# Performance work log

Measured on AMD Instinct MI355X. Metric: run time of the kernel, lower is better.

Reference implementation:

```python
import jax, jax.numpy as jnp
import numpy as np

Q_HEADS, KV_HEADS, HEAD_SIZE, H, MAX_LEN = 16, 4, 64, 1024, 4096
B, S = 1, 4096


def _rope_tables(max_len, head_size):
    half = head_size // 2
    inv_freq = 1.0 / (10000.0 ** (np.arange(half, dtype=np.float32) / half))
    pos = np.arange(max_len, dtype=np.float32)
    ang = pos[:, None] * inv_freq[None, :]  # [max_len, half]
    return jnp.asarray(np.sin(ang)), jnp.asarray(np.cos(ang))


def setup_inputs() -> dict:
    key = jax.random.key(0)
    ks = jax.random.split(key, 6)
    sc = 1.0 / np.sqrt(H)
    x = jax.random.normal(ks[0], (B, S, H), dtype=jnp.float32)
    wq = jax.random.normal(ks[1], (H, H), dtype=jnp.float32) * sc
    wk = jax.random.normal(ks[2], (H, KV_HEADS * HEAD_SIZE), dtype=jnp.float32) * sc
    wv = jax.random.normal(ks[3], (H, KV_HEADS * HEAD_SIZE), dtype=jnp.float32) * sc
    wo = jax.random.normal(ks[4], (H, H), dtype=jnp.float32) * sc
    sin, cos = _rope_tables(MAX_LEN, HEAD_SIZE)
    full_mask = jnp.tril(jnp.ones((MAX_LEN, MAX_LEN), dtype=bool))
    attention_mask = jnp.ones((B, S), dtype=jnp.int32)
    return {"x": x, "attention_mask": attention_mask, "start": 0,
            "wq": wq, "wk": wk, "wv": wv, "wo": wo,
            "sin": sin, "cos": cos, "full_mask": full_mask}


def _rotate(t, sin, cos, start):
    # t: [b, heads, s, head_size]; interleaved even/odd RoPE
    s = t.shape[2]
    sn = sin[start:start + s, :][None, None, :, :]
    cs = cos[start:start + s, :][None, None, :, :]
    even, odd = t[..., 0::2], t[..., 1::2]
    out_even = cs * even - sn * odd
    out_odd = sn * even + cs * odd
    return jnp.stack((out_even, out_odd), axis=-1).reshape(t.shape)


def _expand_kv(t, group):
    # [b, kv_heads, s, d] -> [b, kv_heads*group, s, d]
    b, kvh, s, d = t.shape
    return jnp.broadcast_to(t[:, :, None], (b, kvh, group, s, d)).reshape(b, kvh * group, s, d)


def reference(x, attention_mask, start, wq, wk, wv, wo, sin, cos, full_mask):
    b, s, _ = x.shape
    group = Q_HEADS // KV_HEADS
    Q = (x @ wq).reshape(b, s, Q_HEADS, HEAD_SIZE).transpose(0, 2, 1, 3)
    K = (x @ wk).reshape(b, s, KV_HEADS, HEAD_SIZE).transpose(0, 2, 1, 3)
    V = (x @ wv).reshape(b, s, KV_HEADS, HEAD_SIZE).transpose(0, 2, 1, 3)
    Q = _rotate(Q, sin, cos, start)
    K = _rotate(K, sin, cos, start)
    K = _expand_kv(K, group)
    V = _expand_kv(V, group)
    z = jnp.einsum('bhqd,bhkd->bhqk', Q, K) / (HEAD_SIZE ** 0.5)
    kv_len = start + s
    mask = full_mask[:s, :kv_len][None, None, :, :]
    amask = (attention_mask[:, :kv_len] != 0)[:, None, None, :]
    mask = mask & amask
    z = jnp.where(mask, z, -1000000.0)
    A = jax.nn.softmax(z, axis=-1)
    ctx = jnp.einsum('bhqk,bhkd->bhqd', A, V)
    q_mask = attention_mask[:, :s].astype(ctx.dtype)[:, None, :, None]
    ctx = ctx * q_mask
    ctx = ctx.transpose(0, 2, 1, 3).reshape(b, s, H)
    return ctx @ wo
```

## Files before the change

### kernel.cpp

```cpp
#include <hip/hip_runtime.h>

typedef __bf16 bf16x8 __attribute__((ext_vector_type(8)));
typedef float f32x4 __attribute__((ext_vector_type(4)));
typedef unsigned int u32x4 __attribute__((ext_vector_type(4)));

typedef const void __attribute__((address_space(1)))* gas1;
typedef void __attribute__((address_space(3)))* las3;

__device__ __forceinline__ unsigned short f2bf(float f) {
  unsigned int u = __builtin_bit_cast(unsigned int, f);
  u += 0x7fffu + ((u >> 16) & 1u);
  return (unsigned short)(u >> 16);
}
__device__ __forceinline__ float bf2f(unsigned short h) {
  unsigned int u = ((unsigned int)h) << 16;
  return __builtin_bit_cast(float, u);
}
__device__ __forceinline__ unsigned int pack2bf(float lo, float hi) {
  return (unsigned int)f2bf(lo) | ((unsigned int)f2bf(hi) << 16);
}
__device__ __forceinline__ unsigned int packtr(float lo, float hi) {
  return __builtin_amdgcn_perm(__builtin_bit_cast(unsigned int, hi),
                               __builtin_bit_cast(unsigned int, lo), 0x07060302u);
}

__global__ __launch_bounds__(256) void cvt_f32_bf16(const float* __restrict__ src,
                                                    unsigned short* __restrict__ dst, int n4) {
  int i = blockIdx.x * 256 + threadIdx.x;
  if (i >= n4) return;
  float4 v = ((const float4*)src)[i];
  uint2 o;
  o.x = pack2bf(v.x, v.y);
  o.y = pack2bf(v.z, v.w);
  ((uint2*)dst)[i] = o;
}

__global__ __launch_bounds__(256) void transpose_cvt(const float* __restrict__ src,
                                                     unsigned short* __restrict__ dst,
                                                     int R, int C) {
  __shared__ float tile[32][33];
  int c0 = blockIdx.x * 32, r0 = blockIdx.y * 32;
  int tx = threadIdx.x & 31, ty = threadIdx.x >> 5;
#pragma unroll
  for (int i = 0; i < 4; ++i)
    tile[ty + i * 8][tx] = src[(r0 + ty + i * 8) * C + c0 + tx];
  __syncthreads();
#pragma unroll
  for (int i = 0; i < 4; ++i)
    dst[(c0 + ty + i * 8) * R + r0 + tx] = f2bf(tile[tx][ty + i * 8]);
}

__global__ __launch_bounds__(256, 2) void gemm_bt2(const unsigned short* __restrict__ A,
                                                   const unsigned short* __restrict__ Bt,
                                                   void* __restrict__ Cout,
                                                   int M, int N, int K, int outF32) {
  __shared__ __align__(16) unsigned short Als[128 * 32];
  __shared__ __align__(16) unsigned short Bls[128 * 32];
  const int tid = threadIdx.x;
  const int wave = tid >> 6, lane = tid & 63;
  const int lgrp = lane >> 4, lmod = lane & 15;
  const int wm = (wave & 1) * 64, wn = (wave >> 1) * 64;
  const int m0 = blockIdx.y * 128, n0 = blockIdx.x * 128;

  f32x4 acc[4][4] = {};

  for (int k0 = 0; k0 < K; k0 += 32) {
    __syncthreads();
#pragma unroll
    for (int it = 0; it < 2; ++it) {
      int idx = tid + it * 256;
      int rr = idx >> 2, cc = (idx & 3) * 8;
      __builtin_amdgcn_global_load_lds((gas1)(const void*)&A[(size_t)(m0 + rr) * K + k0 + cc],
                                       (las3)(void*)&Als[(it * 256 + wave * 64) * 8], 16, 0, 0);
      __builtin_amdgcn_global_load_lds((gas1)(const void*)&Bt[(size_t)(n0 + rr) * K + k0 + cc],
                                       (las3)(void*)&Bls[(it * 256 + wave * 64) * 8], 16, 0, 0);
    }
    __syncthreads();
    bf16x8 af[4], bfr[4];
#pragma unroll
    for (int mi = 0; mi < 4; ++mi)
      af[mi] = __builtin_bit_cast(bf16x8, *(const u32x4*)&Als[(wm + mi * 16 + lmod) * 32 + lgrp * 8]);
#pragma unroll
    for (int ni = 0; ni < 4; ++ni)
      bfr[ni] = __builtin_bit_cast(bf16x8, *(const u32x4*)&Bls[(wn + ni * 16 + lmod) * 32 + lgrp * 8]);
#pragma unroll
    for (int mi = 0; mi < 4; ++mi)
#pragma unroll
      for (int ni = 0; ni < 4; ++ni)
        acc[mi][ni] = __builtin_amdgcn_mfma_f32_16x16x32_bf16(af[mi], bfr[ni], acc[mi][ni], 0, 0, 0);
  }

#pragma unroll
  for (int mi = 0; mi < 4; ++mi)
#pragma unroll
    for (int ni = 0; ni < 4; ++ni)
#pragma unroll
      for (int r = 0; r < 4; ++r) {
        int row = m0 + wm + mi * 16 + lgrp * 4 + r;
        int col = n0 + wn + ni * 16 + lmod;
        float v = acc[mi][ni][r];
        if (outF32) ((float*)Cout)[row * N + col] = v;
        else ((unsigned short*)Cout)[row * N + col] = f2bf(v);
      }
}

__global__ __launch_bounds__(256) void rope_split(const unsigned short* __restrict__ qkv,
                                                  const float* __restrict__ sinT,
                                                  const float* __restrict__ cosT,
                                                  unsigned short* __restrict__ Qh,
                                                  unsigned short* __restrict__ Kh) {
  const float qscale = 0.18033688011112042f;
  int p = blockIdx.x * 256 + threadIdx.x;
  int s = p / 640, cp = p % 640;
  int col = cp * 2;
  unsigned int pair = *(const unsigned int*)&qkv[s * 1536 + col];
  float e = bf2f((unsigned short)(pair & 0xffff));
  float o = bf2f((unsigned short)(pair >> 16));
  if (col < 1024) {
    int h = col >> 6, d = col & 63, i = d >> 1;
    float sn = sinT[s * 32 + i], cs = cosT[s * 32 + i];
    unsigned int w = pack2bf((cs * e - sn * o) * qscale, (sn * e + cs * o) * qscale);
    *(unsigned int*)&Qh[(h * 4096 + s) * 64 + d] = w;
  } else {
    int c = col - 1024;
    int h = c >> 6, d = c & 63, i = d >> 1;
    float sn = sinT[s * 32 + i], cs = cosT[s * 32 + i];
    unsigned int w = pack2bf(cs * e - sn * o, sn * e + cs * o);
    *(unsigned int*)&Kh[(h * 4096 + s) * 64 + d] = w;
  }
}

__global__ __launch_bounds__(256) void transpose_v(const unsigned short* __restrict__ qkv,
                                                   unsigned short* __restrict__ Vt) {
  __shared__ unsigned short tile[32][33];
  int h = blockIdx.z;
  int d0 = blockIdx.y * 32;
  int s0 = blockIdx.x * 32;
  int tx = threadIdx.x & 31, ty = threadIdx.x >> 5;
#pragma unroll
  for (int i = 0; i < 4; ++i)
    tile[ty + i * 8][tx] = qkv[(s0 + ty + i * 8) * 1536 + 1280 + h * 64 + d0 + tx];
  __syncthreads();
#pragma unroll
  for (int i = 0; i < 4; ++i)
    Vt[(h * 64 + d0 + ty + i * 8) * 4096 + s0 + tx] = tile[tx][ty + i * 8];
}

__global__ __launch_bounds__(256, 2) void attn3(const unsigned short* __restrict__ Qh,
                                                const unsigned short* __restrict__ Kh,
                                                const unsigned short* __restrict__ Vt,
                                                unsigned short* __restrict__ ctx) {
  __shared__ __align__(16) unsigned short Kls[128 * 68];
  __shared__ __align__(16) unsigned short Vls[64 * 136];
  const int bx = blockIdx.x;
  const int head = bx & 15;
  const int qidx = bx >> 4;
  const int qb = (qidx < 16) ? (31 - qidx) : (qidx - 16);
  const int kvh = head >> 2;
  const int tid = threadIdx.x;
  const int wave = tid >> 6, lane = tid & 63;
  const int lgrp = lane >> 4, lmod = lane & 15;
  const int qbase = qb * 128;

  const unsigned short* Kg = Kh + (size_t)kvh * 4096 * 64;
  const unsigned short* Vg = Vt + (size_t)kvh * 64 * 4096;

  bf16x8 qf[2][2];
  int qrow[2];
#pragma unroll
  for (int qt = 0; qt < 2; ++qt) {
    qrow[qt] = qbase + wave * 32 + qt * 16 + lmod;
    const unsigned short* Qg = Qh + ((size_t)head * 4096 + qrow[qt]) * 64;
    qf[qt][0] = __builtin_bit_cast(bf16x8, *(const u32x4*)&Qg[lgrp * 8]);
    qf[qt][1] = __builtin_bit_cast(bf16x8, *(const u32x4*)&Qg[32 + lgrp * 8]);
  }

  const int kbase = (8 * (lmod >> 2) + (lmod & 3)) * 68 + lgrp * 8;
  const int vbase = lmod * 136 + lgrp * 8;

  f32x4 accO[2][4] = {};
  float m_i[2] = {-3e38f, -3e38f}, l_i[2] = {0.f, 0.f};

  for (int kc = 0; kc <= qb; ++kc) {
    const int kb = kc * 128;
    __syncthreads();
#pragma unroll
    for (int i = 0; i < 4; ++i) {
      int ii = tid + i * 256;
      int r = ii >> 3, sg = (ii & 7) * 8;
      u32x4 dK = *(const u32x4*)&Kg[(size_t)(kb + r) * 64 + sg];
      uint2* pd = (uint2*)&Kls[r * 68 + sg];
      pd[0] = make_uint2(dK[0], dK[1]);
      pd[1] = make_uint2(dK[2], dK[3]);
    }
#pragma unroll
    for (int i = 0; i < 4; ++i) {
      int ii = tid + i * 256;
      int r = ii >> 4, sg = (ii & 15) * 8;
      *(u32x4*)&Vls[r * 136 + sg] = *(const u32x4*)&Vg[(size_t)r * 4096 + kb + sg];
    }
    __syncthreads();

    f32x4 s[4][2][2];
#pragma unroll
    for (int g = 0; g < 4; ++g)
#pragma unroll
      for (int t = 0; t < 2; ++t) {
        const unsigned short* ka = &Kls[kbase + (32 * g + 4 * t) * 68];
        uint2 a0 = *(const uint2*)&ka[0];
        uint2 a1 = *(const uint2*)&ka[4];
        uint2 b0 = *(const uint2*)&ka[32];
        uint2 b1 = *(const uint2*)&ka[36];
        u32x4 lo = {a0.x, a0.y, a1.x, a1.y};
        u32x4 hi = {b0.x, b0.y, b1.x, b1.y};
        bf16x8 alo = __builtin_bit_cast(bf16x8, lo);
        bf16x8 ahi = __builtin_bit_cast(bf16x8, hi);
#pragma unroll
        for (int qt = 0; qt < 2; ++qt) {
          f32x4 z = {};
          z = __builtin_amdgcn_mfma_f32_16x16x32_bf16(alo, qf[qt][0], z, 0, 0, 0);
          z = __builtin_amdgcn_mfma_f32_16x16x32_bf16(ahi, qf[qt][1], z, 0, 0, 0);
          s[g][t][qt] = z;
        }
      }

#pragma unroll
    for (int qt = 0; qt < 2; ++qt) {
      if (kb + 127 > qbase + wave * 32 + qt * 16) {
#pragma unroll
        for (int g = 0; g < 4; ++g)
#pragma unroll
          for (int t = 0; t < 2; ++t)
#pragma unroll
            for (int r = 0; r < 4; ++r) {
              int key = kb + 32 * g + 8 * lgrp + 4 * t + r;
              if (key > qrow[qt]) s[g][t][qt][r] = -3e38f;
            }
      }
    }

#pragma unroll
    for (int qt = 0; qt < 2; ++qt) {
      f32x4 v0 = s[0][0][qt], v1 = s[0][1][qt];
#pragma unroll
      for (int g = 1; g < 4; ++g)
#pragma unroll
        for (int r = 0; r < 4; ++r) {
          v0[r] = fmaxf(v0[r], s[g][0][qt][r]);
          v1[r] = fmaxf(v1[r], s[g][1][qt][r]);
        }
      float mx = fmaxf(fmaxf(fmaxf(v0[0], v0[1]), fmaxf(v0[2], v0[3])),
                       fmaxf(fmaxf(v1[0], v1[1]), fmaxf(v1[2], v1[3])));
      mx = fmaxf(mx, __shfl_xor(mx, 16, 64));
      mx = fmaxf(mx, __shfl_xor(mx, 32, 64));
      float mnew = fmaxf(m_i[qt], mx);
      float alpha = __builtin_amdgcn_exp2f(m_i[qt] - mnew);
      m_i[qt] = mnew;
      f32x4 su = {};
#pragma unroll
      for (int g = 0; g < 4; ++g)
#pragma unroll
        for (int t = 0; t < 2; ++t)
#pragma unroll
          for (int r = 0; r < 4; ++r) {
            float ev = __builtin_amdgcn_exp2f(s[g][t][qt][r] - mnew);
            s[g][t][qt][r] = ev;
            su[r] += ev;
          }
      float rs = (su[0] + su[1]) + (su[2] + su[3]);
      rs += __shfl_xor(rs, 16, 64);
      rs += __shfl_xor(rs, 32, 64);
      l_i[qt] = l_i[qt] * alpha + rs;
#pragma unroll
      for (int dt = 0; dt < 4; ++dt)
#pragma unroll
        for (int r = 0; r < 4; ++r) accO[qt][dt][r] *= alpha;
    }

#pragma unroll
    for (int g = 0; g < 4; ++g) {
      bf16x8 pf[2];
#pragma unroll
      for (int qt = 0; qt < 2; ++qt) {
        u32x4 pk;
        pk[0] = packtr(s[g][0][qt][0], s[g][0][qt][1]);
        pk[1] = packtr(s[g][0][qt][2], s[g][0][qt][3]);
        pk[2] = packtr(s[g][1][qt][0], s[g][1][qt][1]);
        pk[3] = packtr(s[g][1][qt][2], s[g][1][qt][3]);
        pf[qt] = __builtin_bit_cast(bf16x8, pk);
      }
#pragma unroll
      for (int dt = 0; dt < 4; ++dt) {
        bf16x8 vf = __builtin_bit_cast(bf16x8, *(const u32x4*)&Vls[vbase + dt * 2176 + 32 * g]);
        accO[0][dt] = __builtin_amdgcn_mfma_f32_16x16x32_bf16(vf, pf[0], accO[0][dt], 0, 0, 0);
        accO[1][dt] = __builtin_amdgcn_mfma_f32_16x16x32_bf16(vf, pf[1], accO[1][dt], 0, 0, 0);
      }
    }
  }

#pragma unroll
  for (int qt = 0; qt < 2; ++qt) {
    float inv = 1.f / l_i[qt];
#pragma unroll
    for (int dt = 0; dt < 4; ++dt) {
      uint2 o;
      o.x = pack2bf(accO[qt][dt][0] * inv, accO[qt][dt][1] * inv);
      o.y = pack2bf(accO[qt][dt][2] * inv, accO[qt][dt][3] * inv);
      *(uint2*)&ctx[(size_t)qrow[qt] * 1024 + head * 64 + dt * 16 + lgrp * 4] = o;
    }
  }
}

extern "C" void kernel_launch(void* const* d_in, const int* in_sizes, int n_in,
                              void* d_out, int out_size, void* d_ws, size_t ws_size,
                              hipStream_t stream) {
  const float* x    = (const float*)d_in[0];
  const float* wq   = (const float*)d_in[3];
  const float* wk   = (const float*)d_in[4];
  const float* wv   = (const float*)d_in[5];
  const float* wo   = (const float*)d_in[6];
  const float* sinT = (const float*)d_in[7];
  const float* cosT = (const float*)d_in[8];

  unsigned short* ws    = (unsigned short*)d_ws;
  unsigned short* xb    = ws;
  unsigned short* wtqkv = xb + 4096 * 1024;
  unsigned short* wot   = wtqkv + 1536 * 1024;
  unsigned short* qkv   = wot + 1024 * 1024;
  unsigned short* Qh    = qkv + 4096 * 1536;
  unsigned short* Kh    = Qh + 16 * 4096 * 64;
  unsigned short* Vt    = Kh + 4 * 4096 * 64;
  unsigned short* ctx   = Vt + 4 * 64 * 4096;
  float* out = (float*)d_out;

  cvt_f32_bf16<<<4096, 256, 0, stream>>>(x, xb, 4096 * 1024 / 4);
  transpose_cvt<<<dim3(32, 32), 256, 0, stream>>>(wq, wtqkv, 1024, 1024);
  transpose_cvt<<<dim3(8, 32), 256, 0, stream>>>(wk, wtqkv + 1024 * 1024, 1024, 256);
  transpose_cvt<<<dim3(8, 32), 256, 0, stream>>>(wv, wtqkv + 1280 * 1024, 1024, 256);
  transpose_cvt<<<dim3(32, 32), 256, 0, stream>>>(wo, wot, 1024, 1024);

  gemm_bt2<<<dim3(12, 32), 256, 0, stream>>>(xb, wtqkv, qkv, 4096, 1536, 1024, 0);

  rope_split<<<10240, 256, 0, stream>>>(qkv, sinT, cosT, Qh, Kh);
  transpose_v<<<dim3(128, 2, 4), 256, 0, stream>>>(qkv, Vt);

  attn3<<<dim3(512), 256, 0, stream>>>(Qh, Kh, Vt, ctx);

  gemm_bt2<<<dim3(8, 32), 256, 0, stream>>>(ctx, wot, out, 4096, 1024, 1024, 1);
}
```

Measured before the change: 269.5 us.

## Split causal attention KV ranges across blocks with combine pass; smaller GEMM tiles

Attention now splits each query block's causal key range into up to four segments, so the grid grows from 512 to 1280 blocks with more even per-block work. A new combine kernel merges the partial outputs using the saved max and sum values. The GEMMs switch to 64x128 tiles with 128-thread blocks to launch more blocks. In exchange, partial results take an extra global write and read, and Opart reuses the xb workspace region.

```diff
diff --git a/kernel.cpp b/kernel.cpp
--- a/kernel.cpp
+++ b/kernel.cpp
@@ -50,17 +50,18 @@
     dst[(c0 + ty + i * 8) * R + r0 + tx] = f2bf(tile[tx][ty + i * 8]);
 }
 
-__global__ __launch_bounds__(256, 2) void gemm_bt2(const unsigned short* __restrict__ A,
-                                                   const unsigned short* __restrict__ Bt,
-                                                   void* __restrict__ Cout,
-                                                   int M, int N, int K, int outF32) {
-  __shared__ __align__(16) unsigned short Als[128 * 32];
+__global__ __launch_bounds__(128) void gemm_bt3(const unsigned short* __restrict__ A,
+                                                const unsigned short* __restrict__ Bt,
+                                                void* __restrict__ Cout,
+                                                int M, int N, int K, int outF32) {
+  __shared__ __align__(16) unsigned short Als[64 * 32];
   __shared__ __align__(16) unsigned short Bls[128 * 32];
   const int tid = threadIdx.x;
   const int wave = tid >> 6, lane = tid & 63;
   const int lgrp = lane >> 4, lmod = lane & 15;
-  const int wm = (wave & 1) * 64, wn = (wave >> 1) * 64;
-  const int m0 = blockIdx.y * 128, n0 = blockIdx.x * 128;
+  const int wn = wave * 64;
+  const int m0 = blockIdx.y * 64, n0 = blockIdx.x * 128;
+  const int lr = lane >> 2, lc = (lane & 3) * 8;
 
   f32x4 acc[4][4] = {};
 
@@ -68,18 +69,23 @@
     __syncthreads();
 #pragma unroll
     for (int it = 0; it < 2; ++it) {
-      int idx = tid + it * 256;
-      int rr = idx >> 2, cc = (idx & 3) * 8;
-      __builtin_amdgcn_global_load_lds((gas1)(const void*)&A[(size_t)(m0 + rr) * K + k0 + cc],
-                                       (las3)(void*)&Als[(it * 256 + wave * 64) * 8], 16, 0, 0);
-      __builtin_amdgcn_global_load_lds((gas1)(const void*)&Bt[(size_t)(n0 + rr) * K + k0 + cc],
-                                       (las3)(void*)&Bls[(it * 256 + wave * 64) * 8], 16, 0, 0);
+      int idx = wave * 2 + it;
+      __builtin_amdgcn_global_load_lds(
+          (gas1)(const void*)&A[(size_t)(m0 + idx * 16 + lr) * K + k0 + lc],
+          (las3)(void*)&Als[idx * 512], 16, 0, 0);
+    }
+#pragma unroll
+    for (int it = 0; it < 4; ++it) {
+      int idx = wave * 4 + it;
+      __builtin_amdgcn_global_load_lds(
+          (gas1)(const void*)&Bt[(size_t)(n0 + idx * 16 + lr) * K + k0 + lc],
+          (las3)(void*)&Bls[idx * 512], 16, 0, 0);
     }
     __syncthreads();
     bf16x8 af[4], bfr[4];
 #pragma unroll
     for (int mi = 0; mi < 4; ++mi)
-      af[mi] = __builtin_bit_cast(bf16x8, *(const u32x4*)&Als[(wm + mi * 16 + lmod) * 32 + lgrp * 8]);
+      af[mi] = __builtin_bit_cast(bf16x8, *(const u32x4*)&Als[(mi * 16 + lmod) * 32 + lgrp * 8]);
 #pragma unroll
     for (int ni = 0; ni < 4; ++ni)
       bfr[ni] = __builtin_bit_cast(bf16x8, *(const u32x4*)&Bls[(wn + ni * 16 + lmod) * 32 + lgrp * 8]);
@@ -96,11 +102,11 @@
     for (int ni = 0; ni < 4; ++ni)
 #pragma unroll
       for (int r = 0; r < 4; ++r) {
-        int row = m0 + wm + mi * 16 + lgrp * 4 + r;
+        int row = m0 + mi * 16 + lgrp * 4 + r;
         int col = n0 + wn + ni * 16 + lmod;
         float v = acc[mi][ni][r];
-        if (outF32) ((float*)Cout)[row * N + col] = v;
-        else ((unsigned short*)Cout)[row * N + col] = f2bf(v);
+        if (outF32) ((float*)Cout)[(size_t)row * N + col] = v;
+        else ((unsigned short*)Cout)[(size_t)row * N + col] = f2bf(v);
       }
 }
 
@@ -146,16 +152,29 @@
     Vt[(h * 64 + d0 + ty + i * 8) * 4096 + s0 + tx] = tile[tx][ty + i * 8];
 }
 
-__global__ __launch_bounds__(256, 2) void attn3(const unsigned short* __restrict__ Qh,
+__global__ __launch_bounds__(256, 2) void attn4(const unsigned short* __restrict__ Qh,
                                                 const unsigned short* __restrict__ Kh,
                                                 const unsigned short* __restrict__ Vt,
-                                                unsigned short* __restrict__ ctx) {
+                                                unsigned short* __restrict__ Opart,
+                                                float2* __restrict__ ML) {
   __shared__ __align__(16) unsigned short Kls[128 * 68];
   __shared__ __align__(16) unsigned short Vls[64 * 136];
-  const int bx = blockIdx.x;
-  const int head = bx & 15;
-  const int qidx = bx >> 4;
-  const int qb = (qidx < 16) ? (31 - qidx) : (qidx - 16);
+  const int head = blockIdx.y;
+  const int r = 79 - blockIdx.x;
+  int g, base;
+  if (r < 8) { g = 0; base = 0; }
+  else if (r < 24) { g = 1; base = 8; }
+  else if (r < 48) { g = 2; base = 24; }
+  else { g = 3; base = 48; }
+  const int ns = g + 1;
+  const int local = r - base;
+  const int qb = 8 * g + local / ns;
+  const int sseg = local % ns;
+  const int nc = qb + 1;
+  const int qq = nc / ns, rem = nc % ns;
+  const int c0 = sseg * qq + (sseg < rem ? sseg : rem);
+  const int cnt = qq + (sseg < rem ? 1 : 0);
+
   const int kvh = head >> 2;
   const int tid = threadIdx.x;
   const int wave = tid >> 6, lane = tid & 63;
@@ -181,32 +200,33 @@
   f32x4 accO[2][4] = {};
   float m_i[2] = {-3e38f, -3e38f}, l_i[2] = {0.f, 0.f};
 
-  for (int kc = 0; kc <= qb; ++kc) {
+  for (int kci = 0; kci < cnt; ++kci) {
+    const int kc = c0 + kci;
     const int kb = kc * 128;
     __syncthreads();
 #pragma unroll
     for (int i = 0; i < 4; ++i) {
       int ii = tid + i * 256;
-      int r = ii >> 3, sg = (ii & 7) * 8;
-      u32x4 dK = *(const u32x4*)&Kg[(size_t)(kb + r) * 64 + sg];
-      uint2* pd = (uint2*)&Kls[r * 68 + sg];
+      int rr = ii >> 3, sg = (ii & 7) * 8;
+      u32x4 dK = *(const u32x4*)&Kg[(size_t)(kb + rr) * 64 + sg];
+      uint2* pd = (uint2*)&Kls[rr * 68 + sg];
       pd[0] = make_uint2(dK[0], dK[1]);
       pd[1] = make_uint2(dK[2], dK[3]);
     }
 #pragma unroll
     for (int i = 0; i < 4; ++i) {
       int ii = tid + i * 256;
-      int r = ii >> 4, sg = (ii & 15) * 8;
-      *(u32x4*)&Vls[r * 136 + sg] = *(const u32x4*)&Vg[(size_t)r * 4096 + kb + sg];
+      int rr = ii >> 4, sg = (ii & 15) * 8;
+      *(u32x4*)&Vls[rr * 136 + sg] = *(const u32x4*)&Vg[(size_t)rr * 4096 + kb + sg];
     }
     __syncthreads();
 
     f32x4 s[4][2][2];
 #pragma unroll
-    for (int g = 0; g < 4; ++g)
+    for (int gg = 0; gg < 4; ++gg)
 #pragma unroll
       for (int t = 0; t < 2; ++t) {
-        const unsigned short* ka = &Kls[kbase + (32 * g + 4 * t) * 68];
+        const unsigned short* ka = &Kls[kbase + (32 * gg + 4 * t) * 68];
         uint2 a0 = *(const uint2*)&ka[0];
         uint2 a1 = *(const uint2*)&ka[4];
         uint2 b0 = *(const uint2*)&ka[32];
@@ -220,34 +240,33 @@
           f32x4 z = {};
           z = __builtin_amdgcn_mfma_f32_16x16x32_bf16(alo, qf[qt][0], z, 0, 0, 0);
           z = __builtin_amdgcn_mfma_f32_16x16x32_bf16(ahi, qf[qt][1], z, 0, 0, 0);
-          s[g][t][qt] = z;
+          s[gg][t][qt] = z;
         }
       }
 
-#pragma unroll
-    for (int qt = 0; qt < 2; ++qt) {
-      if (kb + 127 > qbase + wave * 32 + qt * 16) {
-#pragma unroll
-        for (int g = 0; g < 4; ++g)
+    if (kc == qb) {
+#pragma unroll
+      for (int qt = 0; qt < 2; ++qt)
+#pragma unroll
+        for (int gg = 0; gg < 4; ++gg)
 #pragma unroll
           for (int t = 0; t < 2; ++t)
 #pragma unroll
-            for (int r = 0; r < 4; ++r) {
-              int key = kb + 32 * g + 8 * lgrp + 4 * t + r;
-              if (key > qrow[qt]) s[g][t][qt][r] = -3e38f;
+            for (int rr = 0; rr < 4; ++rr) {
+              int key = kb + 32 * gg + 8 * lgrp + 4 * t + rr;
+              if (key > qrow[qt]) s[gg][t][qt][rr] = -3e38f;
             }
-      }
     }
 
 #pragma unroll
     for (int qt = 0; qt < 2; ++qt) {
       f32x4 v0 = s[0][0][qt], v1 = s[0][1][qt];
 #pragma unroll
-      for (int g = 1; g < 4; ++g)
-#pragma unroll
-        for (int r = 0; r < 4; ++r) {
-          v0[r] = fmaxf(v0[r], s[g][0][qt][r]);
-          v1[r] = fmaxf(v1[r], s[g][1][qt][r]);
+      for (int gg = 1; gg < 4; ++gg)
+#pragma unroll
+        for (int rr = 0; rr < 4; ++rr) {
+          v0[rr] = fmaxf(v0[rr], s[gg][0][qt][rr]);
+          v1[rr] = fmaxf(v1[rr], s[gg][1][qt][rr]);
         }
       float mx = fmaxf(fmaxf(fmaxf(v0[0], v0[1]), fmaxf(v0[2], v0[3])),
                        fmaxf(fmaxf(v1[0], v1[1]), fmaxf(v1[2], v1[3])));
@@ -258,14 +277,14 @@
       m_i[qt] = mnew;
       f32x4 su = {};
 #pragma unroll
-      for (int g = 0; g < 4; ++g)
+      for (int gg = 0; gg < 4; ++gg)
 #pragma unroll
         for (int t = 0; t < 2; ++t)
 #pragma unroll
-          for (int r = 0; r < 4; ++r) {
-            float ev = __builtin_amdgcn_exp2f(s[g][t][qt][r] - mnew);
-            s[g][t][qt][r] = ev;
-            su[r] += ev;
+          for (int rr = 0; rr < 4; ++rr) {
+            float ev = __builtin_amdgcn_exp2f(s[gg][t][qt][rr] - mnew);
+            s[gg][t][qt][rr] = ev;
+            su[rr] += ev;
           }
       float rs = (su[0] + su[1]) + (su[2] + su[3]);
       rs += __shfl_xor(rs, 16, 64);
@@ -274,40 +293,91 @@
 #pragma unroll
       for (int dt = 0; dt < 4; ++dt)
 #pragma unroll
-        for (int r = 0; r < 4; ++r) accO[qt][dt][r] *= alpha;
-    }
-
-#pragma unroll
-    for (int g = 0; g < 4; ++g) {
+        for (int rr = 0; rr < 4; ++rr) accO[qt][dt][rr] *= alpha;
+    }
+
+#pragma unroll
+    for (int gg = 0; gg < 4; ++gg) {
       bf16x8 pf[2];
 #pragma unroll
       for (int qt = 0; qt < 2; ++qt) {
         u32x4 pk;
-        pk[0] = packtr(s[g][0][qt][0], s[g][0][qt][1]);
-        pk[1] = packtr(s[g][0][qt][2], s[g][0][qt][3]);
-        pk[2] = packtr(s[g][1][qt][0], s[g][1][qt][1]);
-        pk[3] = packtr(s[g][1][qt][2], s[g][1][qt][3]);
+        pk[0] = packtr(s[gg][0][qt][0], s[gg][0][qt][1]);
+        pk[1] = packtr(s[gg][0][qt][2], s[gg][0][qt][3]);
+        pk[2] = packtr(s[gg][1][qt][0], s[gg][1][qt][1]);
+        pk[3] = packtr(s[gg][1][qt][2], s[gg][1][qt][3]);
         pf[qt] = __builtin_bit_cast(bf16x8, pk);
       }
 #pragma unroll
       for (int dt = 0; dt < 4; ++dt) {
-        bf16x8 vf = __builtin_bit_cast(bf16x8, *(const u32x4*)&Vls[vbase + dt * 2176 + 32 * g]);
+        bf16x8 vf = __builtin_bit_cast(bf16x8, *(const u32x4*)&Vls[vbase + dt * 2176 + 32 * gg]);
         accO[0][dt] = __builtin_amdgcn_mfma_f32_16x16x32_bf16(vf, pf[0], accO[0][dt], 0, 0, 0);
         accO[1][dt] = __builtin_amdgcn_mfma_f32_16x16x32_bf16(vf, pf[1], accO[1][dt], 0, 0, 0);
       }
     }
   }
 
+  const size_t obase = (size_t)(head * 80 + r) * 128;
 #pragma unroll
   for (int qt = 0; qt < 2; ++qt) {
-    float inv = 1.f / l_i[qt];
+    int lrow = wave * 32 + qt * 16 + lmod;
 #pragma unroll
     for (int dt = 0; dt < 4; ++dt) {
       uint2 o;
-      o.x = pack2bf(accO[qt][dt][0] * inv, accO[qt][dt][1] * inv);
-      o.y = pack2bf(accO[qt][dt][2] * inv, accO[qt][dt][3] * inv);
-      *(uint2*)&ctx[(size_t)qrow[qt] * 1024 + head * 64 + dt * 16 + lgrp * 4] = o;
-    }
+      o.x = pack2bf(accO[qt][dt][0], accO[qt][dt][1]);
+      o.y = pack2bf(accO[qt][dt][2], accO[qt][dt][3]);
+      *(uint2*)&Opart[(obase + lrow) * 64 + dt * 16 + lgrp * 4] = o;
+    }
+  }
+  if (lane < 16) {
+#pragma unroll
+    for (int qt = 0; qt < 2; ++qt) {
+      int lrow = wave * 32 + qt * 16 + lane;
+      ML[obase + lrow] = make_float2(m_i[qt], l_i[qt]);
+    }
+  }
+}
+
+__global__ __launch_bounds__(256) void attn_combine(const unsigned short* __restrict__ Opart,
+                                                    const float2* __restrict__ ML,
+                                                    unsigned short* __restrict__ ctx) {
+  const int qb = blockIdx.x, head = blockIdx.y;
+  const int g = qb >> 3;
+  const int ns = g + 1;
+  const int sbase = 4 * g * (g + 1) + (qb - 8 * g) * (g + 1);
+  const int tid = threadIdx.x;
+  const int d8 = (tid & 7) * 8;
+#pragma unroll
+  for (int pass = 0; pass < 4; ++pass) {
+    int row = (tid >> 3) + pass * 32;
+    float M = -3e38f;
+    float2 mls[4];
+    for (int s = 0; s < ns; ++s) {
+      mls[s] = ML[(size_t)(head * 80 + sbase + s) * 128 + row];
+      M = fmaxf(M, mls[s].x);
+    }
+    float w[4], ltot = 0.f;
+    for (int s = 0; s < ns; ++s) {
+      w[s] = __builtin_amdgcn_exp2f(mls[s].x - M);
+      ltot += w[s] * mls[s].y;
+    }
+    float inv = 1.f / ltot;
+    float acc[8] = {};
+    for (int s = 0; s < ns; ++s) {
+      u32x4 pv = *(const u32x4*)&Opart[((size_t)(head * 80 + sbase + s) * 128 + row) * 64 + d8];
+      float ws = w[s];
+#pragma unroll
+      for (int j = 0; j < 4; ++j) {
+        unsigned int word = pv[j];
+        acc[2 * j]     += ws * bf2f((unsigned short)(word & 0xffff));
+        acc[2 * j + 1] += ws * bf2f((unsigned short)(word >> 16));
+      }
+    }
+    u32x4 o;
+#pragma unroll
+    for (int j = 0; j < 4; ++j)
+      o[j] = pack2bf(acc[2 * j] * inv, acc[2 * j + 1] * inv);
+    *(u32x4*)&ctx[(size_t)(qb * 128 + row) * 1024 + head * 64 + d8] = o;
   }
 }
 
@@ -325,12 +395,14 @@
   unsigned short* ws    = (unsigned short*)d_ws;
   unsigned short* xb    = ws;
   unsigned short* wtqkv = xb + 4096 * 1024;
-  unsigned short* wot   = wtqkv + 1536 * 1024;
-  unsigned short* qkv   = wot + 1024 * 1024;
+  unsigned short* qkv   = wtqkv + 1536 * 1024;
   unsigned short* Qh    = qkv + 4096 * 1536;
   unsigned short* Kh    = Qh + 16 * 4096 * 64;
   unsigned short* Vt    = Kh + 4 * 4096 * 64;
   unsigned short* ctx   = Vt + 4 * 64 * 4096;
+  unsigned short* wot   = ctx + 4096 * 1024;
+  unsigned short* Opart = ws;
+  float2*         ML    = (float2*)(ws + 16 * 80 * 128 * 64);
   float* out = (float*)d_out;
 
   cvt_f32_bf16<<<4096, 256, 0, stream>>>(x, xb, 4096 * 1024 / 4);
@@ -339,12 +411,13 @@
   transpose_cvt<<<dim3(8, 32), 256, 0, stream>>>(wv, wtqkv + 1280 * 1024, 1024, 256);
   transpose_cvt<<<dim3(32, 32), 256, 0, stream>>>(wo, wot, 1024, 1024);
 
-  gemm_bt2<<<dim3(12, 32), 256, 0, stream>>>(xb, wtqkv, qkv, 4096, 1536, 1024, 0);
+  gemm_bt3<<<dim3(12, 64), 128, 0, stream>>>(xb, wtqkv, qkv, 4096, 1536, 1024, 0);
 
   rope_split<<<10240, 256, 0, stream>>>(qkv, sinT, cosT, Qh, Kh);
   transpose_v<<<dim3(128, 2, 4), 256, 0, stream>>>(qkv, Vt);
 
-  attn3<<<dim3(512), 256, 0, stream>>>(Qh, Kh, Vt, ctx);
-
-  gemm_bt2<<<dim3(8, 32), 256, 0, stream>>>(ctx, wot, out, 4096, 1024, 1024, 1);
-}
+  attn4<<<dim3(80, 16), 256, 0, stream>>>(Qh, Kh, Vt, Opart, ML);
+  attn_combine<<<dim3(32, 16), 256, 0, stream>>>(Opart, ML, ctx);
+
+  gemm_bt3<<<dim3(8, 64), 128, 0, stream>>>(ctx, wot, out, 4096, 1024, 1024, 1);
+}
```

Result: slower. 305.2 us (+13.3%).
